# Performance work log

Hardware: AMD Instinct MI355X
Metric: run time of the kernel (lower is better)

## Reference

```python
import jax, jax.numpy as jnp
import numpy as np

MAX_VALUE = 127.0  # signed 8-bit: 2**(8-1)-1


def _quantize_int8(t, amax):
    # per-tensor symmetric quantization: round(x * 127/amax), clamped to [-127, 127]
    scale = MAX_VALUE / amax
    return jnp.clip(jnp.round(t * scale), -MAX_VALUE, MAX_VALUE).astype(jnp.int8)


def setup_inputs() -> dict:
    key = jax.random.key(0)
    k1, k2, k3 = jax.random.split(key, 3)
    N, K, M = 8192, 4096, 4096
    x = jax.random.normal(k1, (N, K), dtype=jnp.float32)
    weight = jax.random.normal(k2, (M, K), dtype=jnp.float32) * (1.0 / np.sqrt(K))
    bias = jax.random.normal(k3, (M,), dtype=jnp.float32) * (1.0 / np.sqrt(K))
    return {"x": x, "weight": weight, "bias": bias}


def reference(x, weight, bias):
    # amax from max-abs calibration (per-tensor), as TensorQuantizer would hold
    amax = jnp.max(jnp.abs(x))
    amax_w = jnp.max(jnp.abs(weight))
    qi = _quantize_int8(x, amax)          # [N, K] int8
    qw = _quantize_int8(weight, amax_w)   # [M, K] int8
    acc = jnp.matmul(qi.astype(jnp.int32), qw.astype(jnp.int32).T)  # [N, M] int32
    # dequant: output / ((max/amax) * (max/amax_w)), then bias
    dequant = (amax * amax_w) / (MAX_VALUE * MAX_VALUE)
    return acc.astype(jnp.float32) * dequant + bias
```

## Files before the change

kernel.cpp:

```cpp
#include <hip/hip_runtime.h>

#define K_DIM 4096
#define N_DIM 8192
#define M_DIM 4096

typedef int v4i __attribute__((ext_vector_type(4)));

__global__ void amax2_kernel(const float4* __restrict__ x,
                             const float4* __restrict__ w,
                             unsigned* __restrict__ scal) {
  float m0 = 0.f, m1 = 0.f;
  unsigned* out;
  if (blockIdx.x < 2048) {
    const long base = (long)blockIdx.x * 256 + threadIdx.x;
#pragma unroll
    for (int k = 0; k < 16; k += 2) {
      float4 a = x[base + (long)k * 524288];
      float4 b = x[base + (long)(k + 1) * 524288];
      m0 = fmaxf(m0, fmaxf(fmaxf(fabsf(a.x), fabsf(a.y)),
                           fmaxf(fabsf(a.z), fabsf(a.w))));
      m1 = fmaxf(m1, fmaxf(fmaxf(fabsf(b.x), fabsf(b.y)),
                           fmaxf(fabsf(b.z), fabsf(b.w))));
    }
    out = scal + 0;
  } else {
    const long base = (long)(blockIdx.x - 2048) * 256 + threadIdx.x;
#pragma unroll
    for (int k = 0; k < 16; k += 2) {
      float4 a = w[base + (long)k * 262144];
      float4 b = w[base + (long)(k + 1) * 262144];
      m0 = fmaxf(m0, fmaxf(fmaxf(fabsf(a.x), fabsf(a.y)),
                           fmaxf(fabsf(a.z), fabsf(a.w))));
      m1 = fmaxf(m1, fmaxf(fmaxf(fabsf(b.x), fabsf(b.y)),
                           fmaxf(fabsf(b.z), fabsf(b.w))));
    }
    out = scal + 1;
  }
  float m = fmaxf(m0, m1);
#pragma unroll
  for (int off = 32; off > 0; off >>= 1)
    m = fmaxf(m, __shfl_down(m, off));
  __shared__ float sm[4];
  int lane = threadIdx.x & 63, wv = threadIdx.x >> 6;
  if (lane == 0) sm[wv] = m;
  __syncthreads();
  if (threadIdx.x == 0) {
    m = fmaxf(fmaxf(sm[0], sm[1]), fmaxf(sm[2], sm[3]));
    atomicMax(out, __float_as_uint(m));
  }
}

__device__ __forceinline__ unsigned pack4(float4 v, float s) {
  int q0 = (int)fminf(fmaxf(rintf(v.x * s), -127.f), 127.f);
  int q1 = (int)fminf(fmaxf(rintf(v.y * s), -127.f), 127.f);
  int q2 = (int)fminf(fmaxf(rintf(v.z * s), -127.f), 127.f);
  int q3 = (int)fminf(fmaxf(rintf(v.w * s), -127.f), 127.f);
  return (unsigned)(q0 & 255) | ((unsigned)(q1 & 255) << 8) |
         ((unsigned)(q2 & 255) << 16) | ((unsigned)(q3 & 255) << 24);
}

__global__ void quant2_kernel(const float4* __restrict__ x,
                              const float4* __restrict__ w,
                              unsigned* __restrict__ qx, unsigned* __restrict__ qw,
                              const unsigned* __restrict__ scal) {
  if (blockIdx.x < 2048) {
    const float s = 127.0f / __uint_as_float(scal[0]);
    const long base = (long)blockIdx.x * 256 + threadIdx.x;
#pragma unroll
    for (int k = 0; k < 16; ++k)
      qx[base + (long)k * 524288] = pack4(x[base + (long)k * 524288], s);
  } else {
    const float s = 127.0f / __uint_as_float(scal[1]);
    const long base = (long)(blockIdx.x - 2048) * 256 + threadIdx.x;
#pragma unroll
    for (int k = 0; k < 16; ++k)
      qw[base + (long)k * 262144] = pack4(w[base + (long)k * 262144], s);
  }
}

__device__ __forceinline__ void gld_lds16(const void* g, void* l) {
  __builtin_amdgcn_global_load_lds(
      (const __attribute__((address_space(1))) void*)g,
      (__attribute__((address_space(3))) void*)l, 16, 0, 0);
}

__global__ __launch_bounds__(512, 2) void gemm_i8(
    const signed char* __restrict__ A,
    const signed char* __restrict__ B,
    const float* __restrict__ bias,
    float* __restrict__ out,
    const unsigned* __restrict__ scal)
{
  __shared__ signed char lds[4][2][128 * 128];

  const int tid = threadIdx.x;
  const int lane = tid & 63;
  const int w = tid >> 6;
  const int wm = w >> 2;
  const int wn = w & 3;

  const int bid = blockIdx.x;
  const int xcd = bid & 7, idx = bid >> 3;
  const int bx = (xcd & 3) * 8 + (idx & 7);
  const int by = (xcd >> 2) * 8 + (idx >> 3);
  const long r0 = (long)bx * 256;
  const long c0 = (long)by * 256;

  const int u = (tid & 7) ^ ((tid >> 3) & 7);
  const long sR = (long)(u >> 2) * 128 + (tid >> 3);
  const int scol = (u & 3) * 16;
  const signed char* gA = A + (r0 + sR) * K_DIM + scol;
  const signed char* gB = B + (c0 + sR) * K_DIM + scol;
  const int ldst = tid * 16;

  v4i acc[8][4];
#pragma unroll
  for (int i = 0; i < 8; ++i)
#pragma unroll
    for (int j = 0; j < 4; ++j) acc[i][j] = (v4i){0, 0, 0, 0};

  const int fr = lane & 15;
  const int fq = lane >> 4;
  const int sw = fr & 7;

  const int aoff = fr * 128 + (((wm << 2) | fq) ^ sw) * 16;
  const int boff = ((wn & 1) * 64 + fr) * 128 + ((((wn >> 1) << 2) | fq) ^ sw) * 16;

  auto STAGE = [&](int T, int p) {
    signed char* la = &lds[T & 3][0][0];
    signed char* lb = &lds[T & 3][1][0];
    gld_lds16(gA + (long)p * 64 * K_DIM + T * 64, la + p * 8192 + ldst);
    gld_lds16(gB + (long)p * 64 * K_DIM + T * 64, lb + p * 8192 + ldst);
  };

  auto TILE = [&](int T, bool stg, int guard) {
    if (guard == 8) asm volatile("s_waitcnt vmcnt(8)" ::: "memory");
    else if (guard == 4) asm volatile("s_waitcnt vmcnt(4)" ::: "memory");
    else asm volatile("s_waitcnt vmcnt(0)" ::: "memory");
    __builtin_amdgcn_s_barrier();
    const signed char* la = &lds[T & 3][0][0];
    const signed char* lb = &lds[T & 3][1][0];
    v4i bv[4], av[8];
#pragma unroll
    for (int nf = 0; nf < 4; ++nf)
      bv[nf] = *(const v4i*)(lb + boff + nf * 2048);
#pragma unroll
    for (int mi = 0; mi < 4; ++mi)
      av[mi] = *(const v4i*)(la + aoff + mi * 2048);
#pragma unroll
    for (int mi = 0; mi < 4; ++mi)
      av[4 + mi] = *(const v4i*)(la + aoff + 8192 + mi * 2048);
    if (stg) { STAGE(T + 3, 0); STAGE(T + 3, 1); }
    __builtin_amdgcn_s_setprio(1);
#pragma unroll
    for (int mi = 0; mi < 8; ++mi)
#pragma unroll
      for (int nf = 0; nf < 4; ++nf)
        acc[mi][nf] = __builtin_amdgcn_mfma_i32_16x16x64_i8(av[mi], bv[nf],
                                                            acc[mi][nf], 0, 0, 0);
    __builtin_amdgcn_s_setprio(0);
  };

  const int NT = K_DIM / 64;
#pragma unroll
  for (int T = 0; T < 3; ++T) { STAGE(T, 0); STAGE(T, 1); }

#pragma unroll 1
  for (int T = 0; T < NT - 3; ++T) TILE(T, true, 8);
  TILE(NT - 3, false, 8);
  TILE(NT - 2, false, 4);
  TILE(NT - 1, false, 0);

  const float dq =
      (__uint_as_float(scal[0]) * __uint_as_float(scal[1])) / 16129.0f;
  float bs[4];
#pragma unroll
  for (int nf = 0; nf < 4; ++nf) bs[nf] = bias[c0 + wn * 64 + nf * 16 + fr];

#pragma unroll
  for (int mf = 0; mf < 8; ++mf) {
    const long rbase = r0 + wm * 128 + mf * 16 + fq * 4;
#pragma unroll
    for (int nf = 0; nf < 4; ++nf) {
      const long c = c0 + wn * 64 + nf * 16 + fr;
#pragma unroll
      for (int t = 0; t < 4; ++t) {
        out[(rbase + t) * (long)M_DIM + c] = (float)acc[mf][nf][t] * dq + bs[nf];
      }
    }
  }
}

extern "C" void kernel_launch(void* const* d_in, const int* in_sizes, int n_in,
                              void* d_out, int out_size, void* d_ws, size_t ws_size,
                              hipStream_t stream) {
  const float* x = (const float*)d_in[0];
  const float* wt = (const float*)d_in[1];
  const float* bias = (const float*)d_in[2];
  float* out = (float*)d_out;

  unsigned* scal = (unsigned*)d_ws;
  signed char* qx = (signed char*)d_ws + 256;
  signed char* qw = qx + (long)N_DIM * K_DIM;

  hipMemsetAsync(d_ws, 0, 16, stream);

  amax2_kernel<<<3072, 256, 0, stream>>>((const float4*)x, (const float4*)wt,
                                         scal);
  quant2_kernel<<<3072, 256, 0, stream>>>((const float4*)x, (const float4*)wt,
                                          (unsigned*)qx, (unsigned*)qw, scal);

  gemm_i8<<<512, 512, 0, stream>>>(qx, qw, bias, out, scal);
}
```

Before: 435.1 us.

## Fuse amax and quantize via cooperative grid sync; use 256-thread GEMM blocks

Replaces the separate amax and quantize kernels with one cooperative kernel that reduces max-abs, synchronizes the grid, then quantizes. This saves a launch and may let the second read of the inputs hit cache. The GEMM moves from 8 waves of 128x64 sub-tiles to 4 waves of 128x128 sub-tiles per 256x256 block. That doubles the accumulator registers per wave and limits occupancy to one block, while staging loads are issued before the LDS fragment reads. Risks include register pressure or spills with 64 accumulator vectors, and weaker latency hiding with fewer waves.

```diff
diff --git a/kernel.cpp b/kernel.cpp
--- a/kernel.cpp
+++ b/kernel.cpp
@@ -1,54 +1,13 @@
 #include <hip/hip_runtime.h>
+#include <hip/hip_cooperative_groups.h>
+
+namespace cg = cooperative_groups;
 
 #define K_DIM 4096
 #define N_DIM 8192
 #define M_DIM 4096
 
 typedef int v4i __attribute__((ext_vector_type(4)));
-
-__global__ void amax2_kernel(const float4* __restrict__ x,
-                             const float4* __restrict__ w,
-                             unsigned* __restrict__ scal) {
-  float m0 = 0.f, m1 = 0.f;
-  unsigned* out;
-  if (blockIdx.x < 2048) {
-    const long base = (long)blockIdx.x * 256 + threadIdx.x;
-#pragma unroll
-    for (int k = 0; k < 16; k += 2) {
-      float4 a = x[base + (long)k * 524288];
-      float4 b = x[base + (long)(k + 1) * 524288];
-      m0 = fmaxf(m0, fmaxf(fmaxf(fabsf(a.x), fabsf(a.y)),
-                           fmaxf(fabsf(a.z), fabsf(a.w))));
-      m1 = fmaxf(m1, fmaxf(fmaxf(fabsf(b.x), fabsf(b.y)),
-                           fmaxf(fabsf(b.z), fabsf(b.w))));
-    }
-    out = scal + 0;
-  } else {
-    const long base = (long)(blockIdx.x - 2048) * 256 + threadIdx.x;
-#pragma unroll
-    for (int k = 0; k < 16; k += 2) {
-      float4 a = w[base + (long)k * 262144];
-      float4 b = w[base + (long)(k + 1) * 262144];
-      m0 = fmaxf(m0, fmaxf(fmaxf(fabsf(a.x), fabsf(a.y)),
-                           fmaxf(fabsf(a.z), fabsf(a.w))));
-      m1 = fmaxf(m1, fmaxf(fmaxf(fabsf(b.x), fabsf(b.y)),
-                           fmaxf(fabsf(b.z), fabsf(b.w))));
-    }
-    out = scal + 1;
-  }
-  float m = fmaxf(m0, m1);
-#pragma unroll
-  for (int off = 32; off > 0; off >>= 1)
-    m = fmaxf(m, __shfl_down(m, off));
-  __shared__ float sm[4];
-  int lane = threadIdx.x & 63, wv = threadIdx.x >> 6;
-  if (lane == 0) sm[wv] = m;
-  __syncthreads();
-  if (threadIdx.x == 0) {
-    m = fmaxf(fmaxf(sm[0], sm[1]), fmaxf(sm[2], sm[3]));
-    atomicMax(out, __float_as_uint(m));
-  }
-}
 
 __device__ __forceinline__ unsigned pack4(float4 v, float s) {
   int q0 = (int)fminf(fmaxf(rintf(v.x * s), -127.f), 127.f);
@@ -59,23 +18,49 @@
          ((unsigned)(q2 & 255) << 16) | ((unsigned)(q3 & 255) << 24);
 }
 
-__global__ void quant2_kernel(const float4* __restrict__ x,
-                              const float4* __restrict__ w,
-                              unsigned* __restrict__ qx, unsigned* __restrict__ qw,
-                              const unsigned* __restrict__ scal) {
-  if (blockIdx.x < 2048) {
-    const float s = 127.0f / __uint_as_float(scal[0]);
-    const long base = (long)blockIdx.x * 256 + threadIdx.x;
-#pragma unroll
-    for (int k = 0; k < 16; ++k)
-      qx[base + (long)k * 524288] = pack4(x[base + (long)k * 524288], s);
-  } else {
-    const float s = 127.0f / __uint_as_float(scal[1]);
-    const long base = (long)(blockIdx.x - 2048) * 256 + threadIdx.x;
-#pragma unroll
-    for (int k = 0; k < 16; ++k)
-      qw[base + (long)k * 262144] = pack4(w[base + (long)k * 262144], s);
-  }
+__global__ __launch_bounds__(256, 4) void amaxquant_kernel(
+    const float4* __restrict__ x, const float4* __restrict__ w,
+    unsigned* __restrict__ qx, unsigned* __restrict__ qw,
+    unsigned* __restrict__ scal) {
+  const long xb = (long)blockIdx.x * 16384 + threadIdx.x;
+  const long wb = (long)blockIdx.x * 8192 + threadIdx.x;
+  float m0 = 0.f, m1 = 0.f;
+#pragma unroll 4
+  for (int k = 0; k < 64; ++k) {
+    float4 v = x[xb + (long)k * 256];
+    m0 = fmaxf(m0, fmaxf(fmaxf(fabsf(v.x), fabsf(v.y)),
+                         fmaxf(fabsf(v.z), fabsf(v.w))));
+  }
+#pragma unroll 4
+  for (int k = 0; k < 32; ++k) {
+    float4 v = w[wb + (long)k * 256];
+    m1 = fmaxf(m1, fmaxf(fmaxf(fabsf(v.x), fabsf(v.y)),
+                         fmaxf(fabsf(v.z), fabsf(v.w))));
+  }
+#pragma unroll
+  for (int off = 32; off > 0; off >>= 1) {
+    m0 = fmaxf(m0, __shfl_down(m0, off));
+    m1 = fmaxf(m1, __shfl_down(m1, off));
+  }
+  __shared__ float s0[4], s1[4];
+  const int lane = threadIdx.x & 63, wv = threadIdx.x >> 6;
+  if (lane == 0) { s0[wv] = m0; s1[wv] = m1; }
+  __syncthreads();
+  if (threadIdx.x == 0) {
+    atomicMax(scal + 0, __float_as_uint(fmaxf(fmaxf(s0[0], s0[1]),
+                                              fmaxf(s0[2], s0[3]))));
+    atomicMax(scal + 1, __float_as_uint(fmaxf(fmaxf(s1[0], s1[1]),
+                                              fmaxf(s1[2], s1[3]))));
+  }
+  cg::this_grid().sync();
+  const float sx = 127.0f / __uint_as_float(scal[0]);
+  const float sw = 127.0f / __uint_as_float(scal[1]);
+#pragma unroll 4
+  for (int k = 0; k < 64; ++k)
+    qx[xb + (long)k * 256] = pack4(x[xb + (long)k * 256], sx);
+#pragma unroll 4
+  for (int k = 0; k < 32; ++k)
+    qw[wb + (long)k * 256] = pack4(w[wb + (long)k * 256], sw);
 }
 
 __device__ __forceinline__ void gld_lds16(const void* g, void* l) {
@@ -84,7 +69,7 @@
       (__attribute__((address_space(3))) void*)l, 16, 0, 0);
 }
 
-__global__ __launch_bounds__(512, 2) void gemm_i8(
+__global__ __launch_bounds__(256, 1) void gemm_i8(
     const signed char* __restrict__ A,
     const signed char* __restrict__ B,
     const float* __restrict__ bias,
@@ -96,8 +81,8 @@
   const int tid = threadIdx.x;
   const int lane = tid & 63;
   const int w = tid >> 6;
-  const int wm = w >> 2;
-  const int wn = w & 3;
+  const int wm = w >> 1;
+  const int wn = w & 1;
 
   const int bid = blockIdx.x;
   const int xcd = bid & 7, idx = bid >> 3;
@@ -113,79 +98,80 @@
   const signed char* gB = B + (c0 + sR) * K_DIM + scol;
   const int ldst = tid * 16;
 
-  v4i acc[8][4];
+  v4i acc[8][8];
 #pragma unroll
   for (int i = 0; i < 8; ++i)
 #pragma unroll
-    for (int j = 0; j < 4; ++j) acc[i][j] = (v4i){0, 0, 0, 0};
+    for (int j = 0; j < 8; ++j) acc[i][j] = (v4i){0, 0, 0, 0};
 
   const int fr = lane & 15;
   const int fq = lane >> 4;
-  const int sw = fr & 7;
-
-  const int aoff = fr * 128 + (((wm << 2) | fq) ^ sw) * 16;
-  const int boff = ((wn & 1) * 64 + fr) * 128 + ((((wn >> 1) << 2) | fq) ^ sw) * 16;
-
-  auto STAGE = [&](int T, int p) {
+  const int sk = fr & 7;
+
+  const int aoff = fr * 128 + (((wm << 2) | fq) ^ sk) * 16;
+  const int boff = fr * 128 + (((wn << 2) | fq) ^ sk) * 16;
+
+  auto STAGE = [&](int T) {
     signed char* la = &lds[T & 3][0][0];
     signed char* lb = &lds[T & 3][1][0];
-    gld_lds16(gA + (long)p * 64 * K_DIM + T * 64, la + p * 8192 + ldst);
-    gld_lds16(gB + (long)p * 64 * K_DIM + T * 64, lb + p * 8192 + ldst);
+    const long ko = (long)T * 64;
+#pragma unroll
+    for (int p = 0; p < 4; ++p) {
+      gld_lds16(gA + (long)p * 32 * K_DIM + ko, la + p * 4096 + ldst);
+      gld_lds16(gB + (long)p * 32 * K_DIM + ko, lb + p * 4096 + ldst);
+    }
   };
 
   auto TILE = [&](int T, bool stg, int guard) {
-    if (guard == 8) asm volatile("s_waitcnt vmcnt(8)" ::: "memory");
-    else if (guard == 4) asm volatile("s_waitcnt vmcnt(4)" ::: "memory");
+    if (guard == 16) asm volatile("s_waitcnt vmcnt(16)" ::: "memory");
+    else if (guard == 8) asm volatile("s_waitcnt vmcnt(8)" ::: "memory");
     else asm volatile("s_waitcnt vmcnt(0)" ::: "memory");
     __builtin_amdgcn_s_barrier();
+    if (stg) STAGE(T + 3);
     const signed char* la = &lds[T & 3][0][0];
     const signed char* lb = &lds[T & 3][1][0];
-    v4i bv[4], av[8];
-#pragma unroll
-    for (int nf = 0; nf < 4; ++nf)
+    v4i bv[8], av[8];
+#pragma unroll
+    for (int nf = 0; nf < 8; ++nf)
       bv[nf] = *(const v4i*)(lb + boff + nf * 2048);
 #pragma unroll
-    for (int mi = 0; mi < 4; ++mi)
+    for (int mi = 0; mi < 8; ++mi)
       av[mi] = *(const v4i*)(la + aoff + mi * 2048);
-#pragma unroll
-    for (int mi = 0; mi < 4; ++mi)
-      av[4 + mi] = *(const v4i*)(la + aoff + 8192 + mi * 2048);
-    if (stg) { STAGE(T + 3, 0); STAGE(T + 3, 1); }
     __builtin_amdgcn_s_setprio(1);
 #pragma unroll
     for (int mi = 0; mi < 8; ++mi)
 #pragma unroll
-      for (int nf = 0; nf < 4; ++nf)
+      for (int nf = 0; nf < 8; ++nf)
         acc[mi][nf] = __builtin_amdgcn_mfma_i32_16x16x64_i8(av[mi], bv[nf],
                                                             acc[mi][nf], 0, 0, 0);
     __builtin_amdgcn_s_setprio(0);
   };
 
   const int NT = K_DIM / 64;
-#pragma unroll
-  for (int T = 0; T < 3; ++T) { STAGE(T, 0); STAGE(T, 1); }
-
+  STAGE(0);
+  STAGE(1);
+  STAGE(2);
 #pragma unroll 1
-  for (int T = 0; T < NT - 3; ++T) TILE(T, true, 8);
-  TILE(NT - 3, false, 8);
-  TILE(NT - 2, false, 4);
+  for (int T = 0; T < NT - 3; ++T) TILE(T, true, 16);
+  TILE(NT - 3, false, 16);
+  TILE(NT - 2, false, 8);
   TILE(NT - 1, false, 0);
 
   const float dq =
       (__uint_as_float(scal[0]) * __uint_as_float(scal[1])) / 16129.0f;
-  float bs[4];
-#pragma unroll
-  for (int nf = 0; nf < 4; ++nf) bs[nf] = bias[c0 + wn * 64 + nf * 16 + fr];
-
-#pragma unroll
-  for (int mf = 0; mf < 8; ++mf) {
-    const long rbase = r0 + wm * 128 + mf * 16 + fq * 4;
-#pragma unroll
-    for (int nf = 0; nf < 4; ++nf) {
-      const long c = c0 + wn * 64 + nf * 16 + fr;
+  float bs[8];
+#pragma unroll
+  for (int nf = 0; nf < 8; ++nf) bs[nf] = bias[c0 + wn * 128 + nf * 16 + fr];
+
+#pragma unroll
+  for (int mi = 0; mi < 8; ++mi) {
+    const long rbase = r0 + wm * 128 + mi * 16 + fq * 4;
+#pragma unroll
+    for (int nf = 0; nf < 8; ++nf) {
+      const long c = c0 + wn * 128 + nf * 16 + fr;
 #pragma unroll
       for (int t = 0; t < 4; ++t) {
-        out[(rbase + t) * (long)M_DIM + c] = (float)acc[mf][nf][t] * dq + bs[nf];
+        out[(rbase + t) * (long)M_DIM + c] = (float)acc[mi][nf][t] * dq + bs[nf];
       }
     }
   }
@@ -205,10 +191,14 @@
 
   hipMemsetAsync(d_ws, 0, 16, stream);
 
-  amax2_kernel<<<3072, 256, 0, stream>>>((const float4*)x, (const float4*)wt,
-                                         scal);
-  quant2_kernel<<<3072, 256, 0, stream>>>((const float4*)x, (const float4*)wt,
-                                          (unsigned*)qx, (unsigned*)qw, scal);
-
-  gemm_i8<<<512, 512, 0, stream>>>(qx, qw, bias, out, scal);
-}
+  const float4* x4 = (const float4*)x;
+  const float4* w4 = (const float4*)wt;
+  unsigned* qxu = (unsigned*)qx;
+  unsigned* qwu = (unsigned*)qw;
+  void* args[] = {(void*)&x4, (void*)&w4, (void*)&qxu, (void*)&qwu,
+                  (void*)&scal};
+  hipLaunchCooperativeKernel((const void*)amaxquant_kernel, dim3(512),
+                             dim3(256), args, 0, stream);
+
+  gemm_i8<<<512, 256, 0, stream>>>(qx, qw, bias, out, scal);
+}
```

Measured after the change: 507.7 us. +16.7%, slower.
